# Performance work log

Hardware: AMD Instinct MI355X
Metric: run time of the kernel (lower is better)

## Reference

```python
import jax, jax.numpy as jnp
import numpy as np
from jax import lax

B, S, MAXW, D, V, L = 32, 1024, 256, 512, 32000, 2


def setup_inputs() -> dict:
    key = jax.random.key(0)
    ks = jax.random.split(key, 10)
    x = jax.random.randint(ks[0], (B, S), 0, V)
    labels = jax.random.randint(ks[1], (B, MAXW), 0, 2)
    token_word_id = jnp.sort(
        jax.random.randint(ks[2], (B, S), 0, MAXW), axis=-1
    ).astype(jnp.int32)
    s = 1.0 / np.sqrt(D).astype(np.float32)
    emb = (jax.random.normal(ks[3], (V, D), dtype=jnp.float32) * 0.02).at[0].set(0.0)
    W_ih = jax.random.uniform(ks[4], (L, 4 * D, D), minval=-s, maxval=s, dtype=jnp.float32)
    W_hh = jax.random.uniform(ks[5], (L, 4 * D, D), minval=-s, maxval=s, dtype=jnp.float32)
    b_ih = jax.random.uniform(ks[6], (L, 4 * D), minval=-s, maxval=s, dtype=jnp.float32)
    b_hh = jax.random.uniform(ks[7], (L, 4 * D), minval=-s, maxval=s, dtype=jnp.float32)
    W_out = jax.random.uniform(ks[8], (2, D), minval=-s, maxval=s, dtype=jnp.float32)
    b_out = jax.random.uniform(ks[9], (2,), minval=-s, maxval=s, dtype=jnp.float32)
    return dict(x=x, labels=labels, token_word_id=token_word_id, emb=emb,
                W_ih=W_ih, W_hh=W_hh, b_ih=b_ih, b_hh=b_hh,
                W_out=W_out, b_out=b_out)


def _lstm_layer(xs, Wih, Whh, bih, bhh):
    # xs: [B, S, Din]; torch gate order: i, f, g, o
    H = Whh.shape[1]
    x_proj = jnp.einsum('bsd,gd->bsg', xs, Wih) + bih + bhh  # [B,S,4H]
    h0 = jnp.zeros((xs.shape[0], H), xs.dtype)
    c0 = jnp.zeros((xs.shape[0], H), xs.dtype)

    def step(carry, xt):
        h, c = carry
        gates = xt + h @ Whh.T
        i, f, g, o = jnp.split(gates, 4, axis=-1)
        i = jax.nn.sigmoid(i)
        f = jax.nn.sigmoid(f)
        g = jnp.tanh(g)
        o = jax.nn.sigmoid(o)
        c = f * c + i * g
        h = o * jnp.tanh(c)
        return (h, c), h

    _, hs = lax.scan(step, (h0, c0), x_proj.transpose(1, 0, 2))  # [S,B,H]
    return hs.transpose(1, 0, 2)


def reference(x, labels, token_word_id, emb, W_ih, W_hh, b_ih, b_hh, W_out, b_out):
    h = emb[x]  # [B,S,D]
    for l in range(L):
        h = _lstm_layer(h, W_ih[l], W_hh[l], b_ih[l], b_hh[l])
    # ragged token->word mean pooling (segment mean over flattened batch*word ids)
    seg = (jnp.arange(B, dtype=jnp.int32)[:, None] * MAXW + token_word_id).reshape(-1)
    flat = h.reshape(B * S, D)
    sums = jax.ops.segment_sum(flat, seg, num_segments=B * MAXW)
    cnts = jax.ops.segment_sum(jnp.ones((B * S,), h.dtype), seg, num_segments=B * MAXW)
    pooled = jnp.where(cnts[:, None] > 0, sums / jnp.maximum(cnts, 1.0)[:, None], 0.0)
    # span head (dropout is identity in eval)
    logits = pooled @ W_out.T + b_out            # [B*MAXW, 2]
    logp = jax.nn.log_softmax(logits, axis=-1)
    lab = labels.reshape(-1)
    loss = -jnp.mean(jnp.take_along_axis(logp, lab[:, None], axis=1))
    return logits, loss
```

## Files before the change

### kernel.cpp

```cpp
#include <hip/hip_runtime.h>
#include <hip/hip_fp16.h>

typedef unsigned short u16;
typedef unsigned int u32;
typedef unsigned long long u64;
typedef short s16x8 __attribute__((ext_vector_type(8)));
typedef float f32x4 __attribute__((ext_vector_type(4)));

#define BB   32
#define SS   1024
#define DD   512
#define G4   2048
#define MAXW 256
#define NWG  32
#define RING 8
#define HS   (BB*DD)

__device__ __forceinline__ u16 f2bf(float f){
  unsigned int u = __float_as_uint(f);
  u += 0x7fff + ((u >> 16) & 1);
  return (u16)(u >> 16);
}
__device__ __forceinline__ float bf2f(u16 h){
  return __uint_as_float(((unsigned int)h) << 16);
}
__device__ __forceinline__ float sigm(float x){ return 1.f/(1.f + __expf(-x)); }
__device__ __forceinline__ float ftanh(float x){
  float ax = fabsf(x);
  float e = __expf(-2.f*ax);
  float t = (1.f - e)/(1.f + e);
  return copysignf(t, x);
}

__global__ void k_prep(const float* __restrict__ Wih, const float* __restrict__ Whh,
                       const float* __restrict__ bih, const float* __restrict__ bhh,
                       u16* __restrict__ Wih_b, u16* __restrict__ Whh_b,
                       float* __restrict__ biasp){
  long i = (long)blockIdx.x*blockDim.x + threadIdx.x;
  long n = 2l*G4*DD;
  long stride = (long)gridDim.x*blockDim.x;
  for (long k = i; k < n; k += stride){
    Wih_b[k] = f2bf(Wih[k]);
    Whh_b[k] = f2bf(Whh[k]);
  }
  for (long k = i; k < 2*G4; k += stride){
    int lyr = (int)(k / G4), nn = (int)(k % G4);
    int col = nn >> 2, q = nn & 3;
    int g = q*DD + col;
    biasp[k] = bih[lyr*G4 + g] + bhh[lyr*G4 + g];
  }
}

__global__ void k_embed(const int* __restrict__ x, const float* __restrict__ emb,
                        u16* __restrict__ out){
  int bs = blockIdx.x;
  int tok = x[bs];
  const float* src = emb + (size_t)tok * DD;
  u16* dst = out + (size_t)bs * DD;
  for (int d = threadIdx.x; d < DD; d += blockDim.x) dst[d] = f2bf(src[d]);
}

__device__ __forceinline__ void wait2(const u32* p1, u32 n1,
                                      const u32* p2, u32 n2, int& budget){
  if (n1 == 0u && n2 == 0u) return;
  while (budget > 0){
    u32 v1 = n1 ? __hip_atomic_load(p1, __ATOMIC_RELAXED, __HIP_MEMORY_SCOPE_AGENT)
                : 0xffffffffu;
    u32 v2 = n2 ? __hip_atomic_load(p2, __ATOMIC_RELAXED, __HIP_MEMORY_SCOPE_AGENT)
                : 0xffffffffu;
    int ok = (v1 >= n1) && (v2 >= n2);
    if (__all(ok)) break;
    budget--;
    __builtin_amdgcn_s_sleep(1);
  }
}

__device__ __forceinline__ void stage_h(const u16* slab, char* lds, int tid){
  u64 d[16];
  #pragma unroll
  for (int j = 0; j < 16; j++)
    d[j] = __hip_atomic_load((const u64*)slab + j*256 + tid,
                             __ATOMIC_RELAXED, __HIP_MEMORY_SCOPE_AGENT);
  #pragma unroll
  for (int j = 0; j < 16; j++){
    int e = j*256 + tid;
    int b = e >> 7, c8 = e & 127;
    *(u64*)(lds + b*1024 + ((c8*8) ^ ((b & 7) << 4))) = d[j];
  }
}

__device__ __forceinline__ void lds_write16(char* lds, int tid, const u64* d){
  #pragma unroll
  for (int j = 0; j < 16; j++){
    int e = j*256 + tid;
    int b = e >> 7, c8 = e & 127;
    *(u64*)(lds + b*1024 + ((c8*8) ^ ((b & 7) << 4))) = d[j];
  }
}

#define FRAG_BYT(kk) ((lane & 15)*1024 + (((kk)*64 + (lane>>4)*16) ^ (((lane & 15) & 7) << 4)))

__global__ __launch_bounds__(256, 1) void k_recur2(
    const u16* __restrict__ h_io,
    const u16* __restrict__ Wih_b,
    const u16* __restrict__ Whh_b,
    const float* __restrict__ biasp,
    u16* __restrict__ h1r,
    u16* __restrict__ h2r,
    u32* __restrict__ flags,
    u16* __restrict__ h_seq2){
  __shared__ char hX[32768];
  __shared__ char hH[32768];
  const int tid = threadIdx.x;
  const int lane = tid & 63, wv = tid >> 6;
  const int wg = blockIdx.x;
  const bool isL2 = wg >= NWG;
  const int id = wg & (NWG - 1);

  u32* c1 = flags;
  u32* c2 = flags + 64;

  const int pa = id*64 + wv*16 + (lane & 15);
  const size_t arow = (size_t)((pa & 3)*DD + (pa >> 2))*DD;
  const int koff = (lane >> 4)*8;
  const size_t lyrOff = isL2 ? (size_t)G4*DD : 0;
  s16x8 ahh[16], aih[16];
  #pragma unroll
  for (int kk = 0; kk < 16; kk++){
    ahh[kk] = *(const s16x8*)(Whh_b + lyrOff + arow + kk*32 + koff);
    aih[kk] = *(const s16x8*)(Wih_b + lyrOff + arow + kk*32 + koff);
  }
  #pragma unroll
  for (int kk = 0; kk < 16; kk++){
    asm volatile("" : "+v"(ahh[kk]));
    asm volatile("" : "+v"(aih[kk]));
  }

  const int oc = id*16 + wv*4 + (lane >> 4);
  const int cl = wv*4 + (lane >> 4);
  const int b0 = lane & 15, b1 = b0 + 16;
  const f32x4 b4 = *(const f32x4*)(biasp + (isL2 ? G4 : 0) + oc*4);
  float c0 = 0.f, cst1 = 0.f;
  int budget = 1 << 22;

  if (!isL2){
    for (int t = 0; t < SS; t++){
      u64 xd[16];
      #pragma unroll
      for (int j = 0; j < 16; j++){
        int e = j*256 + tid;
        xd[j] = *((const u64*)h_io + ((size_t)(e >> 7)*SS + t)*128 + (e & 127));
      }
      lds_write16(hX, tid, xd);
      __syncthreads();
      f32x4 e0 = {0.f,0.f,0.f,0.f}, e1 = {0.f,0.f,0.f,0.f};
      #pragma unroll
      for (int kk = 0; kk < 16; kk++){
        int byt = FRAG_BYT(kk);
        s16x8 f0 = *(const s16x8*)(hX + byt);
        s16x8 f1 = *(const s16x8*)(hX + byt + 16*1024);
        e0 = __builtin_amdgcn_mfma_f32_16x16x32_bf16(aih[kk], f0, e0, 0, 0, 0);
        e1 = __builtin_amdgcn_mfma_f32_16x16x32_bf16(aih[kk], f1, e1, 0, 0, 0);
      }
      u32 n1 = (t > 0) ? (u32)(NWG*t) : 0u;
      u32 n2 = (t >= RING) ? (u32)(NWG*(t - RING + 1)) : 0u;
      wait2(c1, n1, c2, n2, budget);
      if (t > 0){
        stage_h(h1r + (size_t)((t-1) & (RING-1))*HS, hH, tid);
        __syncthreads();
        #pragma unroll
        for (int kk = 0; kk < 16; kk++){
          int byt = FRAG_BYT(kk);
          s16x8 f0 = *(const s16x8*)(hH + byt);
          s16x8 f1 = *(const s16x8*)(hH + byt + 16*1024);
          e0 = __builtin_amdgcn_mfma_f32_16x16x32_bf16(ahh[kk], f0, e0, 0, 0, 0);
          e1 = __builtin_amdgcn_mfma_f32_16x16x32_bf16(ahh[kk], f1, e1, 0, 0, 0);
        }
      }
      float ig = sigm (e0[0] + b4[0]), fg = sigm (e0[1] + b4[1]);
      float gg = ftanh(e0[2] + b4[2]), og = sigm (e0[3] + b4[3]);
      c0 = fg*c0 + ig*gg;
      float hv0 = og * ftanh(c0);
      ig = sigm (e1[0] + b4[0]); fg = sigm (e1[1] + b4[1]);
      gg = ftanh(e1[2] + b4[2]); og = sigm (e1[3] + b4[3]);
      cst1 = fg*cst1 + ig*gg;
      float hv1 = og * ftanh(cst1);
      u16 hh0 = f2bf(hv0), hh1 = f2bf(hv1);
      u32 p0 = (u32)hh0 | (((u32)__shfl((int)hh0, (lane + 16) & 63) & 0xffffu) << 16);
      u32 p1 = (u32)hh1 | (((u32)__shfl((int)hh1, (lane + 16) & 63) & 0xffffu) << 16);
      u16* dst = h1r + (size_t)(t & (RING-1))*HS;
      if (((lane >> 4) & 1) == 0){
        __hip_atomic_store((u32*)(dst + (size_t)b0*DD + oc), p0,
                           __ATOMIC_RELAXED, __HIP_MEMORY_SCOPE_AGENT);
        __hip_atomic_store((u32*)(dst + (size_t)b1*DD + oc), p1,
                           __ATOMIC_RELAXED, __HIP_MEMORY_SCOPE_AGENT);
      }
      asm volatile("s_waitcnt vmcnt(0)" ::: "memory");
      __syncthreads();
      if (tid == 0) atomicAdd(c1, 1u);
    }
  } else {
    for (int t = 0; t < SS; t++){
      u64 d1[16], d2[16];
      wait2(c1, (u32)(NWG*(t+1)), c2, 0u, budget);
      {
        const u64* s1 = (const u64*)(h1r + (size_t)(t & (RING-1))*HS);
        #pragma unroll
        for (int j = 0; j < 16; j++)
          d1[j] = __hip_atomic_load(s1 + j*256 + tid,
                                    __ATOMIC_RELAXED, __HIP_MEMORY_SCOPE_AGENT);
      }
      if (t > 0){
        wait2(c2, (u32)(NWG*t), c2, 0u, budget);
        const u64* s2 = (const u64*)(h2r + (size_t)((t-1) & 1)*HS);
        #pragma unroll
        for (int j = 0; j < 16; j++)
          d2[j] = __hip_atomic_load(s2 + j*256 + tid,
                                    __ATOMIC_RELAXED, __HIP_MEMORY_SCOPE_AGENT);
      }
      f32x4 e0 = {0.f,0.f,0.f,0.f}, e1 = {0.f,0.f,0.f,0.f};
      lds_write16(hX, tid, d1);
      __syncthreads();
      #pragma unroll
      for (int kk = 0; kk < 16; kk++){
        int byt = FRAG_BYT(kk);
        s16x8 f0 = *(const s16x8*)(hX + byt);
        s16x8 f1 = *(const s16x8*)(hX + byt + 16*1024);
        e0 = __builtin_amdgcn_mfma_f32_16x16x32_bf16(aih[kk], f0, e0, 0, 0, 0);
        e1 = __builtin_amdgcn_mfma_f32_16x16x32_bf16(aih[kk], f1, e1, 0, 0, 0);
      }
      if (t > 0){
        lds_write16(hH, tid, d2);
        __syncthreads();
        #pragma unroll
        for (int kk = 0; kk < 16; kk++){
          int byt = FRAG_BYT(kk);
          s16x8 f0 = *(const s16x8*)(hH + byt);
          s16x8 f1 = *(const s16x8*)(hH + byt + 16*1024);
          e0 = __builtin_amdgcn_mfma_f32_16x16x32_bf16(ahh[kk], f0, e0, 0, 0, 0);
          e1 = __builtin_amdgcn_mfma_f32_16x16x32_bf16(ahh[kk], f1, e1, 0, 0, 0);
        }
      }
      float ig = sigm (e0[0] + b4[0]), fg = sigm (e0[1] + b4[1]);
      float gg = ftanh(e0[2] + b4[2]), og = sigm (e0[3] + b4[3]);
      c0 = fg*c0 + ig*gg;
      float hv0 = og * ftanh(c0);
      ig = sigm (e1[0] + b4[0]); fg = sigm (e1[1] + b4[1]);
      gg = ftanh(e1[2] + b4[2]); og = sigm (e1[3] + b4[3]);
      cst1 = fg*cst1 + ig*gg;
      float hv1 = og * ftanh(cst1);
      u16 hh0 = f2bf(hv0), hh1 = f2bf(hv1);
      u32 p0 = (u32)hh0 | (((u32)__shfl((int)hh0, (lane + 16) & 63) & 0xffffu) << 16);
      u32 p1 = (u32)hh1 | (((u32)__shfl((int)hh1, (lane + 16) & 63) & 0xffffu) << 16);
      u16* dst = h2r + (size_t)(t & 1)*HS;
      if (((lane >> 4) & 1) == 0){
        __hip_atomic_store((u32*)(dst + (size_t)b0*DD + oc), p0,
                           __ATOMIC_RELAXED, __HIP_MEMORY_SCOPE_AGENT);
        __hip_atomic_store((u32*)(dst + (size_t)b1*DD + oc), p1,
                           __ATOMIC_RELAXED, __HIP_MEMORY_SCOPE_AGENT);
      }
      asm volatile("s_waitcnt vmcnt(0)" ::: "memory");
      __syncthreads();
      if (tid == 0) atomicAdd(c2, 1u);
      if (((lane >> 4) & 1) == 0){
        u32* hs = (u32*)h_seq2 + (size_t)t*(HS/2) + id*256;
        hs[b0*8 + (cl >> 1)] = p0;
        hs[b1*8 + (cl >> 1)] = p1;
      }
    }
  }
}

__global__ __launch_bounds__(64) void k_pool(const u16* __restrict__ h_seq,
                                             const int* __restrict__ twid,
                                             const float* __restrict__ Wout,
                                             const float* __restrict__ bout,
                                             float* __restrict__ out){
  int bw = blockIdx.x;
  int b = bw >> 8, w = bw & 255;
  const int* tw = twid + b*SS;
  __shared__ int s_lo, s_hi;
  if (threadIdx.x == 0){
    int l = 0, r = SS;
    while (l < r){ int m = (l + r) >> 1; if (tw[m] < w) l = m + 1; else r = m; }
    s_lo = l;
    r = SS;
    while (l < r){ int m = (l + r) >> 1; if (tw[m] < w + 1) l = m + 1; else r = m; }
    s_hi = l;
  }
  __syncthreads();
  int lo = s_lo, hi = s_hi, cnt = hi - lo;
  int lane = threadIdx.x;
  float p0 = 0.f, p1 = 0.f;
  if (cnt > 0){
    const char* hs = (const char*)h_seq;
    const size_t lo_off = (size_t)(lane >> 1)*1024 + (size_t)b*32 + (lane & 1)*16;
    float sum[8] = {0.f,0.f,0.f,0.f,0.f,0.f,0.f,0.f};
    for (int t = lo; t < hi; t++){
      int4 v = *(const int4*)(hs + (size_t)t*32768 + lo_off);
      const u16* u = (const u16*)&v;
      #pragma unroll
      for (int j = 0; j < 8; j++) sum[j] += bf2f(u[j]);
    }
    float inv = 1.f/(float)cnt;
    #pragma unroll
    for (int j = 0; j < 8; j++){
      float pv = sum[j]*inv;
      int d = lane*8 + j;
      p0 += pv * Wout[d];
      p1 += pv * Wout[DD + d];
    }
  }
  #pragma unroll
  for (int off = 32; off; off >>= 1){
    p0 += __shfl_down(p0, off);
    p1 += __shfl_down(p1, off);
  }
  if (lane == 0){
    out[bw*2 + 0] = p0 + bout[0];
    out[bw*2 + 1] = p1 + bout[1];
  }
}

__global__ __launch_bounds__(256) void k_loss(const float* __restrict__ logits,
                                              const int* __restrict__ labels,
                                              float* __restrict__ out_loss){
  __shared__ float red[256];
  float acc = 0.f;
  for (int i = threadIdx.x; i < BB*MAXW; i += 256){
    float z0 = logits[i*2], z1 = logits[i*2 + 1];
    float m = fmaxf(z0, z1);
    float lse = m + __logf(__expf(z0 - m) + __expf(z1 - m));
    float zl = labels[i] ? z1 : z0;
    acc += (lse - zl);
  }
  red[threadIdx.x] = acc;
  __syncthreads();
  for (int s2 = 128; s2; s2 >>= 1){
    if (threadIdx.x < s2) red[threadIdx.x] += red[threadIdx.x + s2];
    __syncthreads();
  }
  if (threadIdx.x == 0) out_loss[0] = red[0] / (float)(BB*MAXW);
}

extern "C" void kernel_launch(void* const* d_in, const int* in_sizes, int n_in,
                              void* d_out, int out_size, void* d_ws, size_t ws_size,
                              hipStream_t stream){
  (void)in_sizes; (void)n_in; (void)out_size; (void)ws_size;
  const int*   x      = (const int*)  d_in[0];
  const int*   labels = (const int*)  d_in[1];
  const int*   twid   = (const int*)  d_in[2];
  const float* emb    = (const float*)d_in[3];
  const float* Wih    = (const float*)d_in[4];
  const float* Whh    = (const float*)d_in[5];
  const float* bih    = (const float*)d_in[6];
  const float* bhh    = (const float*)d_in[7];
  const float* Wout   = (const float*)d_in[8];
  const float* bout   = (const float*)d_in[9];
  float* out = (float*)d_out;

  char* ws = (char*)d_ws;
  size_t off = 0;
  u16*   h_io   = (u16*)  (ws + off); off += (size_t)BB*SS*DD*2;
  u16*   h_seq2 = (u16*)  (ws + off); off += (size_t)BB*SS*DD*2;
  u16*   Wih_b  = (u16*)  (ws + off); off += (size_t)2*G4*DD*2;
  u16*   Whh_b  = (u16*)  (ws + off); off += (size_t)2*G4*DD*2;
  float* biasp  = (float*)(ws + off); off += (size_t)2*G4*4;
  u16*   h1r    = (u16*)  (ws + off); off += (size_t)RING*HS*2;
  u16*   h2r    = (u16*)  (ws + off); off += (size_t)2*HS*2;
  u32*   flags  = (u32*)  (ws + off); off += 1024;

  k_prep<<<2048, 256, 0, stream>>>(Wih, Whh, bih, bhh, Wih_b, Whh_b, biasp);
  k_embed<<<BB*SS, 256, 0, stream>>>(x, emb, h_io);

  hipMemsetAsync(flags, 0, 1024, stream);

  k_recur2<<<2*NWG, 256, 0, stream>>>(h_io, Wih_b, Whh_b, biasp,
                                      h1r, h2r, flags, h_seq2);

  k_pool<<<BB*MAXW, 64, 0, stream>>>(h_seq2, twid, Wout, bout, out);
  k_loss<<<1, 256, 0, stream>>>(out, labels, out + BB*MAXW*2);
}
```

Measured before the change: 4.307 ms.

## Wavefront-skew both LSTM layers in each workgroup with one shared counter barrier

Replaces the split of 32 layer-1 and 32 layer-2 workgroups with 64 workgroups. In each, two waves compute layer 1 at step k and two waves compute layer 2 at step k-1, coordinated by a single global counter barrier per step. The intent is to cut the two-counter producer/consumer handshakes and halve the per-workgroup slice. It also prefetches the next input row while the barrier is pending. In exchange it removes the 8-deep ring slack, so every step is a hard grid-wide barrier, and every workgroup now stages both hidden states into LDS. The h_seq2 layout and the pooling offsets change to match.

```diff
diff --git a/kernel.cpp b/kernel.cpp
--- a/kernel.cpp
+++ b/kernel.cpp
@@ -12,8 +12,7 @@
 #define DD   512
 #define G4   2048
 #define MAXW 256
-#define NWG  32
-#define RING 8
+#define NWG  64
 #define HS   (BB*DD)
 
 __device__ __forceinline__ u16 f2bf(float f){
@@ -60,32 +59,13 @@
   for (int d = threadIdx.x; d < DD; d += blockDim.x) dst[d] = f2bf(src[d]);
 }
 
-__device__ __forceinline__ void wait2(const u32* p1, u32 n1,
-                                      const u32* p2, u32 n2, int& budget){
-  if (n1 == 0u && n2 == 0u) return;
+__device__ __forceinline__ void waitc(const u32* p, u32 need, int& budget){
+  if (need == 0u) return;
   while (budget > 0){
-    u32 v1 = n1 ? __hip_atomic_load(p1, __ATOMIC_RELAXED, __HIP_MEMORY_SCOPE_AGENT)
-                : 0xffffffffu;
-    u32 v2 = n2 ? __hip_atomic_load(p2, __ATOMIC_RELAXED, __HIP_MEMORY_SCOPE_AGENT)
-                : 0xffffffffu;
-    int ok = (v1 >= n1) && (v2 >= n2);
-    if (__all(ok)) break;
+    u32 v = __hip_atomic_load(p, __ATOMIC_RELAXED, __HIP_MEMORY_SCOPE_AGENT);
+    if (__all((int)(v >= need))) break;
     budget--;
     __builtin_amdgcn_s_sleep(1);
-  }
-}
-
-__device__ __forceinline__ void stage_h(const u16* slab, char* lds, int tid){
-  u64 d[16];
-  #pragma unroll
-  for (int j = 0; j < 16; j++)
-    d[j] = __hip_atomic_load((const u64*)slab + j*256 + tid,
-                             __ATOMIC_RELAXED, __HIP_MEMORY_SCOPE_AGENT);
-  #pragma unroll
-  for (int j = 0; j < 16; j++){
-    int e = j*256 + tid;
-    int b = e >> 7, c8 = e & 127;
-    *(u64*)(lds + b*1024 + ((c8*8) ^ ((b & 7) << 4))) = d[j];
   }
 }
 
@@ -109,21 +89,21 @@
     u16* __restrict__ h2r,
     u32* __restrict__ flags,
     u16* __restrict__ h_seq2){
-  __shared__ char hX[32768];
-  __shared__ char hH[32768];
+  __shared__ char sX [32768];
+  __shared__ char sH1[32768];
+  __shared__ char sH2[32768];
   const int tid = threadIdx.x;
   const int lane = tid & 63, wv = tid >> 6;
   const int wg = blockIdx.x;
-  const bool isL2 = wg >= NWG;
-  const int id = wg & (NWG - 1);
-
-  u32* c1 = flags;
-  u32* c2 = flags + 64;
-
-  const int pa = id*64 + wv*16 + (lane & 15);
+  const bool isL2w = (wv >= 2);
+  const int wvl = wv & 1;
+
+  u32* cc = flags;
+
+  const int pa = wg*32 + wvl*16 + (lane & 15);
   const size_t arow = (size_t)((pa & 3)*DD + (pa >> 2))*DD;
   const int koff = (lane >> 4)*8;
-  const size_t lyrOff = isL2 ? (size_t)G4*DD : 0;
+  const size_t lyrOff = isL2w ? (size_t)G4*DD : 0;
   s16x8 ahh[16], aih[16];
   #pragma unroll
   for (int kk = 0; kk < 16; kk++){
@@ -136,47 +116,92 @@
     asm volatile("" : "+v"(aih[kk]));
   }
 
-  const int oc = id*16 + wv*4 + (lane >> 4);
-  const int cl = wv*4 + (lane >> 4);
+  const int oc = wg*8 + wvl*4 + (lane >> 4);
+  const int cl = wvl*4 + (lane >> 4);
   const int b0 = lane & 15, b1 = b0 + 16;
-  const f32x4 b4 = *(const f32x4*)(biasp + (isL2 ? G4 : 0) + oc*4);
+  const f32x4 b4 = *(const f32x4*)(biasp + (isL2w ? G4 : 0) + oc*4);
   float c0 = 0.f, cst1 = 0.f;
   int budget = 1 << 22;
 
-  if (!isL2){
-    for (int t = 0; t < SS; t++){
-      u64 xd[16];
-      #pragma unroll
-      for (int j = 0; j < 16; j++){
-        int e = j*256 + tid;
-        xd[j] = *((const u64*)h_io + ((size_t)(e >> 7)*SS + t)*128 + (e & 127));
-      }
-      lds_write16(hX, tid, xd);
-      __syncthreads();
-      f32x4 e0 = {0.f,0.f,0.f,0.f}, e1 = {0.f,0.f,0.f,0.f};
+  u64 xd[16];
+  #pragma unroll
+  for (int j = 0; j < 16; j++){
+    int e = j*256 + tid;
+    xd[j] = *((const u64*)h_io + ((size_t)(e >> 7)*SS + 0)*128 + (e & 127));
+  }
+
+  for (int k = 0; k <= SS; k++){
+    waitc(cc, (k > 0) ? (u32)(NWG*k) : 0u, budget);
+    u64 d1[16], d2[16];
+    if (k >= 1){
+      const u64* s1 = (const u64*)(h1r + (size_t)((k-1) & 1)*HS);
+      #pragma unroll
+      for (int j = 0; j < 16; j++)
+        d1[j] = __hip_atomic_load(s1 + j*256 + tid,
+                                  __ATOMIC_RELAXED, __HIP_MEMORY_SCOPE_AGENT);
+    }
+    if (k >= 2){
+      const u64* s2 = (const u64*)(h2r + (size_t)((k-2) & 1)*HS);
+      #pragma unroll
+      for (int j = 0; j < 16; j++)
+        d2[j] = __hip_atomic_load(s2 + j*256 + tid,
+                                  __ATOMIC_RELAXED, __HIP_MEMORY_SCOPE_AGENT);
+    }
+    if (k < SS) lds_write16(sX, tid, xd);
+    __syncthreads();
+    f32x4 e0 = {0.f,0.f,0.f,0.f}, e1 = {0.f,0.f,0.f,0.f};
+    if (!isL2w && k < SS){
       #pragma unroll
       for (int kk = 0; kk < 16; kk++){
         int byt = FRAG_BYT(kk);
-        s16x8 f0 = *(const s16x8*)(hX + byt);
-        s16x8 f1 = *(const s16x8*)(hX + byt + 16*1024);
+        s16x8 f0 = *(const s16x8*)(sX + byt);
+        s16x8 f1 = *(const s16x8*)(sX + byt + 16*1024);
         e0 = __builtin_amdgcn_mfma_f32_16x16x32_bf16(aih[kk], f0, e0, 0, 0, 0);
         e1 = __builtin_amdgcn_mfma_f32_16x16x32_bf16(aih[kk], f1, e1, 0, 0, 0);
       }
-      u32 n1 = (t > 0) ? (u32)(NWG*t) : 0u;
-      u32 n2 = (t >= RING) ? (u32)(NWG*(t - RING + 1)) : 0u;
-      wait2(c1, n1, c2, n2, budget);
-      if (t > 0){
-        stage_h(h1r + (size_t)((t-1) & (RING-1))*HS, hH, tid);
-        __syncthreads();
+    }
+    if (k >= 1){
+      lds_write16(sH1, tid, d1);
+      __syncthreads();
+      if (!isL2w){
+        if (k < SS){
+          #pragma unroll
+          for (int kk = 0; kk < 16; kk++){
+            int byt = FRAG_BYT(kk);
+            s16x8 f0 = *(const s16x8*)(sH1 + byt);
+            s16x8 f1 = *(const s16x8*)(sH1 + byt + 16*1024);
+            e0 = __builtin_amdgcn_mfma_f32_16x16x32_bf16(ahh[kk], f0, e0, 0, 0, 0);
+            e1 = __builtin_amdgcn_mfma_f32_16x16x32_bf16(ahh[kk], f1, e1, 0, 0, 0);
+          }
+        }
+      } else {
         #pragma unroll
         for (int kk = 0; kk < 16; kk++){
           int byt = FRAG_BYT(kk);
-          s16x8 f0 = *(const s16x8*)(hH + byt);
-          s16x8 f1 = *(const s16x8*)(hH + byt + 16*1024);
+          s16x8 f0 = *(const s16x8*)(sH1 + byt);
+          s16x8 f1 = *(const s16x8*)(sH1 + byt + 16*1024);
+          e0 = __builtin_amdgcn_mfma_f32_16x16x32_bf16(aih[kk], f0, e0, 0, 0, 0);
+          e1 = __builtin_amdgcn_mfma_f32_16x16x32_bf16(aih[kk], f1, e1, 0, 0, 0);
+        }
+      }
+    }
+    if (k >= 2){
+      lds_write16(sH2, tid, d2);
+      __syncthreads();
+      if (isL2w){
+        #pragma unroll
+        for (int kk = 0; kk < 16; kk++){
+          int byt = FRAG_BYT(kk);
+          s16x8 f0 = *(const s16x8*)(sH2 + byt);
+          s16x8 f1 = *(const s16x8*)(sH2 + byt + 16*1024);
           e0 = __builtin_amdgcn_mfma_f32_16x16x32_bf16(ahh[kk], f0, e0, 0, 0, 0);
           e1 = __builtin_amdgcn_mfma_f32_16x16x32_bf16(ahh[kk], f1, e1, 0, 0, 0);
         }
       }
+    }
+    const bool act = (!isL2w) ? (k < SS) : (k >= 1);
+    u32 p0 = 0, p1 = 0;
+    if (act){
       float ig = sigm (e0[0] + b4[0]), fg = sigm (e0[1] + b4[1]);
       float gg = ftanh(e0[2] + b4[2]), og = sigm (e0[3] + b4[3]);
       c0 = fg*c0 + ig*gg;
@@ -186,86 +211,30 @@
       cst1 = fg*cst1 + ig*gg;
       float hv1 = og * ftanh(cst1);
       u16 hh0 = f2bf(hv0), hh1 = f2bf(hv1);
-      u32 p0 = (u32)hh0 | (((u32)__shfl((int)hh0, (lane + 16) & 63) & 0xffffu) << 16);
-      u32 p1 = (u32)hh1 | (((u32)__shfl((int)hh1, (lane + 16) & 63) & 0xffffu) << 16);
-      u16* dst = h1r + (size_t)(t & (RING-1))*HS;
+      p0 = (u32)hh0 | (((u32)__shfl((int)hh0, (lane + 16) & 63) & 0xffffu) << 16);
+      p1 = (u32)hh1 | (((u32)__shfl((int)hh1, (lane + 16) & 63) & 0xffffu) << 16);
+      u16* dst = (!isL2w) ? (h1r + (size_t)(k & 1)*HS)
+                          : (h2r + (size_t)((k-1) & 1)*HS);
       if (((lane >> 4) & 1) == 0){
         __hip_atomic_store((u32*)(dst + (size_t)b0*DD + oc), p0,
                            __ATOMIC_RELAXED, __HIP_MEMORY_SCOPE_AGENT);
         __hip_atomic_store((u32*)(dst + (size_t)b1*DD + oc), p1,
                            __ATOMIC_RELAXED, __HIP_MEMORY_SCOPE_AGENT);
       }
-      asm volatile("s_waitcnt vmcnt(0)" ::: "memory");
-      __syncthreads();
-      if (tid == 0) atomicAdd(c1, 1u);
-    }
-  } else {
-    for (int t = 0; t < SS; t++){
-      u64 d1[16], d2[16];
-      wait2(c1, (u32)(NWG*(t+1)), c2, 0u, budget);
-      {
-        const u64* s1 = (const u64*)(h1r + (size_t)(t & (RING-1))*HS);
-        #pragma unroll
-        for (int j = 0; j < 16; j++)
-          d1[j] = __hip_atomic_load(s1 + j*256 + tid,
-                                    __ATOMIC_RELAXED, __HIP_MEMORY_SCOPE_AGENT);
-      }
-      if (t > 0){
-        wait2(c2, (u32)(NWG*t), c2, 0u, budget);
-        const u64* s2 = (const u64*)(h2r + (size_t)((t-1) & 1)*HS);
-        #pragma unroll
-        for (int j = 0; j < 16; j++)
-          d2[j] = __hip_atomic_load(s2 + j*256 + tid,
-                                    __ATOMIC_RELAXED, __HIP_MEMORY_SCOPE_AGENT);
-      }
-      f32x4 e0 = {0.f,0.f,0.f,0.f}, e1 = {0.f,0.f,0.f,0.f};
-      lds_write16(hX, tid, d1);
-      __syncthreads();
-      #pragma unroll
-      for (int kk = 0; kk < 16; kk++){
-        int byt = FRAG_BYT(kk);
-        s16x8 f0 = *(const s16x8*)(hX + byt);
-        s16x8 f1 = *(const s16x8*)(hX + byt + 16*1024);
-        e0 = __builtin_amdgcn_mfma_f32_16x16x32_bf16(aih[kk], f0, e0, 0, 0, 0);
-        e1 = __builtin_amdgcn_mfma_f32_16x16x32_bf16(aih[kk], f1, e1, 0, 0, 0);
-      }
-      if (t > 0){
-        lds_write16(hH, tid, d2);
-        __syncthreads();
-        #pragma unroll
-        for (int kk = 0; kk < 16; kk++){
-          int byt = FRAG_BYT(kk);
-          s16x8 f0 = *(const s16x8*)(hH + byt);
-          s16x8 f1 = *(const s16x8*)(hH + byt + 16*1024);
-          e0 = __builtin_amdgcn_mfma_f32_16x16x32_bf16(ahh[kk], f0, e0, 0, 0, 0);
-          e1 = __builtin_amdgcn_mfma_f32_16x16x32_bf16(ahh[kk], f1, e1, 0, 0, 0);
-        }
-      }
-      float ig = sigm (e0[0] + b4[0]), fg = sigm (e0[1] + b4[1]);
-      float gg = ftanh(e0[2] + b4[2]), og = sigm (e0[3] + b4[3]);
-      c0 = fg*c0 + ig*gg;
-      float hv0 = og * ftanh(c0);
-      ig = sigm (e1[0] + b4[0]); fg = sigm (e1[1] + b4[1]);
-      gg = ftanh(e1[2] + b4[2]); og = sigm (e1[3] + b4[3]);
-      cst1 = fg*cst1 + ig*gg;
-      float hv1 = og * ftanh(cst1);
-      u16 hh0 = f2bf(hv0), hh1 = f2bf(hv1);
-      u32 p0 = (u32)hh0 | (((u32)__shfl((int)hh0, (lane + 16) & 63) & 0xffffu) << 16);
-      u32 p1 = (u32)hh1 | (((u32)__shfl((int)hh1, (lane + 16) & 63) & 0xffffu) << 16);
-      u16* dst = h2r + (size_t)(t & 1)*HS;
-      if (((lane >> 4) & 1) == 0){
-        __hip_atomic_store((u32*)(dst + (size_t)b0*DD + oc), p0,
-                           __ATOMIC_RELAXED, __HIP_MEMORY_SCOPE_AGENT);
-        __hip_atomic_store((u32*)(dst + (size_t)b1*DD + oc), p1,
-                           __ATOMIC_RELAXED, __HIP_MEMORY_SCOPE_AGENT);
-      }
-      asm volatile("s_waitcnt vmcnt(0)" ::: "memory");
-      __syncthreads();
-      if (tid == 0) atomicAdd(c2, 1u);
-      if (((lane >> 4) & 1) == 0){
-        u32* hs = (u32*)h_seq2 + (size_t)t*(HS/2) + id*256;
-        hs[b0*8 + (cl >> 1)] = p0;
-        hs[b1*8 + (cl >> 1)] = p1;
+    }
+    asm volatile("s_waitcnt vmcnt(0)" ::: "memory");
+    __syncthreads();
+    if (tid == 0) atomicAdd(cc, 1u);
+    if (isL2w && k >= 1 && ((lane >> 4) & 1) == 0){
+      u32* hs = (u32*)h_seq2 + (size_t)(k-1)*(HS/2) + wg*128;
+      hs[b0*4 + (cl >> 1)] = p0;
+      hs[b1*4 + (cl >> 1)] = p1;
+    }
+    if (k + 1 < SS){
+      #pragma unroll
+      for (int j = 0; j < 16; j++){
+        int e = j*256 + tid;
+        xd[j] = *((const u64*)h_io + ((size_t)(e >> 7)*SS + (k+1))*128 + (e & 127));
       }
     }
   }
@@ -294,7 +263,7 @@
   float p0 = 0.f, p1 = 0.f;
   if (cnt > 0){
     const char* hs = (const char*)h_seq;
-    const size_t lo_off = (size_t)(lane >> 1)*1024 + (size_t)b*32 + (lane & 1)*16;
+    const size_t lo_off = (size_t)lane*512 + (size_t)b*16;
     float sum[8] = {0.f,0.f,0.f,0.f,0.f,0.f,0.f,0.f};
     for (int t = lo; t < hi; t++){
       int4 v = *(const int4*)(hs + (size_t)t*32768 + lo_off);
@@ -366,7 +335,7 @@
   u16*   Wih_b  = (u16*)  (ws + off); off += (size_t)2*G4*DD*2;
   u16*   Whh_b  = (u16*)  (ws + off); off += (size_t)2*G4*DD*2;
   float* biasp  = (float*)(ws + off); off += (size_t)2*G4*4;
-  u16*   h1r    = (u16*)  (ws + off); off += (size_t)RING*HS*2;
+  u16*   h1r    = (u16*)  (ws + off); off += (size_t)2*HS*2;
   u16*   h2r    = (u16*)  (ws + off); off += (size_t)2*HS*2;
   u32*   flags  = (u32*)  (ws + off); off += 1024;
 
@@ -375,8 +344,8 @@
 
   hipMemsetAsync(flags, 0, 1024, stream);
 
-  k_recur2<<<2*NWG, 256, 0, stream>>>(h_io, Wih_b, Whh_b, biasp,
-                                      h1r, h2r, flags, h_seq2);
+  k_recur2<<<NWG, 256, 0, stream>>>(h_io, Wih_b, Whh_b, biasp,
+                                    h1r, h2r, flags, h_seq2);
 
   k_pool<<<BB*MAXW, 64, 0, stream>>>(h_seq2, twid, Wout, bout, out);
   k_loss<<<1, 256, 0, stream>>>(out, labels, out + BB*MAXW*2);
```

After: 6.626 ms. +53.9%, slower.
